# Performance work log

Measured on AMD Instinct MI355X. Metric: run time of the kernel, lower is better.

## Reference

```python
import jax, jax.numpy as jnp
import numpy as np


def setup_inputs() -> dict:
    key = jax.random.key(0)
    k1, k2, k3, k4, k5, k6 = jax.random.split(key, 6)
    Ne, dim_in, dim_out, B, Nr, E = 100000, 128, 128, 4, 8, 200000
    return {
        "H": jax.random.normal(k1, (Ne, dim_in), dtype=jnp.float32),
        "A": jax.random.uniform(k2, (Nr, B), dtype=jnp.float32),
        "V": jax.random.uniform(k3, (B, dim_in, dim_out), dtype=jnp.float32),
        "edge_row": jax.random.randint(k4, (Nr, E), 0, Ne, dtype=jnp.int32),
        "edge_col": jax.random.randint(k5, (Nr, E), 0, Ne, dtype=jnp.int32),
        "edge_val": jax.random.uniform(k6, (Nr, E), dtype=jnp.float32),
    }


def reference(H, A, V, edge_row, edge_col, edge_val):
    # W = einsum('rb,bio->rio', A, V): basis-decomposed relation weights
    Ne = H.shape[0]
    Nr = A.shape[0]
    W = jnp.einsum('rb,bio->rio', A, V)            # [Nr, dim_in, dim_out]
    HxW = jnp.einsum('ni,rio->rno', H, W)          # [Nr, Ne, dim_out]
    # sparse T_r @ HxW_r: gather source rows (cols of T), scale by values,
    # scatter-add into destination rows. Done for all relations at once.
    msgs = HxW[jnp.arange(Nr)[:, None], edge_col] * edge_val[..., None]  # [Nr, E, dim_out]
    out = jax.ops.segment_sum(
        msgs.reshape(-1, msgs.shape[-1]),
        edge_row.reshape(-1),
        num_segments=Ne,
    )  # sum over relations folded into one segment_sum
    return out
```

## Files before the change

### kernel.cpp

```cpp
#include <hip/hip_runtime.h>

typedef __attribute__((ext_vector_type(8))) short short8;
typedef __attribute__((ext_vector_type(4))) float floatx4;

constexpr int DIM   = 128;
constexpr int NB    = 4;
constexpr int NR    = 8;
constexpr int BROWS = 512;
constexpr int BCAP  = 16384;

static __device__ __forceinline__ unsigned short f2bf(float f) {
    unsigned int u = __float_as_uint(f);
    u += 0x7FFFu + ((u >> 16) & 1u);
    return (unsigned short)(u >> 16);
}
static __device__ __forceinline__ float bf_lo(unsigned int h) {
    return __uint_as_float(h << 16);
}
static __device__ __forceinline__ float bf_hi(unsigned int h) {
    return __uint_as_float(h & 0xFFFF0000u);
}

__global__ __launch_bounds__(256) void build_vfrag(
    const float* __restrict__ V, unsigned short* __restrict__ VfragG)
{
    int idx  = blockIdx.x * 256 + threadIdx.x;
    int lane = idx & 63;
    int ks   = (idx >> 6) & 3;
    int ot   = (idx >> 8) & 7;
    int b    = idx >> 11;

    int o  = ot * 16 + (lane & 15);
    int kb = ks * 32 + (lane >> 4) * 8;

    short8 v;
#pragma unroll
    for (int j = 0; j < 8; ++j)
        v[j] = (short)f2bf(V[((size_t)b * DIM + kb + j) * DIM + o]);
    *reinterpret_cast<short8*>(VfragG + (size_t)idx * 8) = v;
}

__global__ __launch_bounds__(256) void build_wfrag(
    const float* __restrict__ A, const float* __restrict__ V,
    unsigned short* __restrict__ Wfrag)
{
    int idx  = blockIdx.x * 256 + threadIdx.x;
    int lane = idx & 63;
    int ks   = (idx >> 6) & 3;
    int ot   = (idx >> 8) & 7;
    int r    = idx >> 11;

    int o     = ot * 16 + (lane & 15);
    int kbase = ks * 32 + (lane >> 4) * 8;

    float a0 = A[r * NB + 0], a1 = A[r * NB + 1];
    float a2 = A[r * NB + 2], a3 = A[r * NB + 3];

    short8 v;
#pragma unroll
    for (int j = 0; j < 8; ++j) {
        int k = kbase + j;
        float w = a0 * V[(0 * DIM + k) * DIM + o]
                + a1 * V[(1 * DIM + k) * DIM + o]
                + a2 * V[(2 * DIM + k) * DIM + o]
                + a3 * V[(3 * DIM + k) * DIM + o];
        v[j] = (short)f2bf(w);
    }
    *reinterpret_cast<short8*>(Wfrag + (size_t)idx * 8) = v;
}

__global__ __launch_bounds__(256) void h_to_bf(
    const float* __restrict__ H, unsigned short* __restrict__ Hbf, int n8)
{
    int i = blockIdx.x * 256 + threadIdx.x;
    if (i >= n8) return;
    const float4* hp = reinterpret_cast<const float4*>(H) + (size_t)i * 2;
    float4 f0 = hp[0];
    float4 f1 = hp[1];
    short8 v;
    v[0] = (short)f2bf(f0.x); v[1] = (short)f2bf(f0.y);
    v[2] = (short)f2bf(f0.z); v[3] = (short)f2bf(f0.w);
    v[4] = (short)f2bf(f1.x); v[5] = (short)f2bf(f1.y);
    v[6] = (short)f2bf(f1.z); v[7] = (short)f2bf(f1.w);
    *reinterpret_cast<short8*>(Hbf + (size_t)i * 8) = v;
}

__global__ __launch_bounds__(256) void bucket_scatter(
    const int* __restrict__ erow, const int* __restrict__ ecol,
    const float* __restrict__ eval, int* __restrict__ bcnt,
    int2* __restrict__ sorted1, int n, int E, int chunk)
{
    __shared__ int cnt[256];
    __shared__ int base[256];
    int t = threadIdx.x;
    cnt[t] = 0;
    __syncthreads();

    int s = blockIdx.x * chunk;
    int e = s + chunk; if (e > n) e = n;

    for (int i = s + t; i < e; i += 256)
        atomicAdd(&cnt[erow[i] >> 9], 1);
    __syncthreads();

    int c = cnt[t];
    base[t] = (c > 0) ? atomicAdd(&bcnt[t], c) : 0;
    cnt[t] = 0;
    __syncthreads();

    for (int i = s + t; i < e; i += 256) {
        int row = erow[i];
        int bkt = row >> 9;
        int rank = atomicAdd(&cnt[bkt], 1);
        int r = (int)((unsigned)i / (unsigned)E);
        int2 m;
        m.x = ((row & (BROWS - 1)) << 20) | (r << 17) | ecol[i];
        m.y = __float_as_int(eval[i]);
        sorted1[(size_t)bkt * BCAP + base[bkt] + rank] = m;
    }
}

__global__ __launch_bounds__(256) void bucket_scan(
    const int* __restrict__ bcnt, int* __restrict__ bstart,
    int* __restrict__ rowStart, int nbuc, int Ne)
{
    __shared__ int sd[256];
    int t = threadIdx.x;
    int c = (t < nbuc) ? bcnt[t] : 0;
    sd[t] = c; __syncthreads();
#pragma unroll
    for (int off = 1; off < 256; off <<= 1) {
        int v = (t >= off) ? sd[t - off] : 0;
        __syncthreads();
        sd[t] += v;
        __syncthreads();
    }
    if (t < nbuc) bstart[t] = sd[t] - c;
    if (t == nbuc - 1) rowStart[Ne] = sd[t];
}

__global__ __launch_bounds__(256) void bucket_sort(
    const int2* __restrict__ sorted1, const int* __restrict__ bcnt,
    const int* __restrict__ bstart, int* __restrict__ rowStart,
    int2* __restrict__ sorted, int Ne)
{
    __shared__ int hcnt[BROWS];
    __shared__ int hoff[BROWS];
    int b = blockIdx.x;
    int t = threadIdx.x;
    hcnt[t] = 0; hcnt[t + 256] = 0;
    __syncthreads();

    int n = bcnt[b];
    const int2* src = sorted1 + (size_t)b * BCAP;

    for (int i = t; i < n; i += 256)
        atomicAdd(&hcnt[(unsigned)src[i].x >> 20], 1);
    __syncthreads();

    if (t == 0) {
        int run = 0;
#pragma unroll 8
        for (int j = 0; j < BROWS; ++j) { hoff[j] = run; run += hcnt[j]; }
    }
    __syncthreads();

    int bs = bstart[b];
    int rs = b * BROWS;
    int nr = Ne - rs; if (nr > BROWS) nr = BROWS;
    for (int j = t; j < nr; j += 256)
        rowStart[rs + j] = bs + hoff[j];

    hcnt[t] = 0; hcnt[t + 256] = 0;
    __syncthreads();

    for (int i = t; i < n; i += 256) {
        int2 m = src[i];
        int lr = (unsigned)m.x >> 20;
        int pos = bs + hoff[lr] + atomicAdd(&hcnt[lr], 1);
        sorted[pos] = m;
    }
}

__global__ __launch_bounds__(256) void agg_kernel(
    const unsigned short* __restrict__ Hbf,
    const int*  __restrict__ rowStart,
    const int2* __restrict__ sorted,
    const float* __restrict__ Aw,
    unsigned short* __restrict__ AggT, int Ne)
{
    int tid  = threadIdx.x;
    int wid  = __builtin_amdgcn_readfirstlane(blockIdx.x * 4 + (tid >> 6));
    if (wid >= Ne) return;
    int lane = tid & 63;

    int s = __builtin_amdgcn_readfirstlane(rowStart[wid]);
    int e = __builtin_amdgcn_readfirstlane(rowStart[wid + 1]);

    const float4* Af = reinterpret_cast<const float4*>(Aw);

    float2 acc[4];
#pragma unroll
    for (int b = 0; b < 4; ++b) { acc[b].x = 0.f; acc[b].y = 0.f; }

    int i = s;
    for (; i + 8 <= e; i += 8) {
        int kk[8];
        float vv[8];
        unsigned int hh[8];
#pragma unroll
        for (int u = 0; u < 8; ++u) {
            int2 m = sorted[i + u];
            kk[u] = __builtin_amdgcn_readfirstlane(m.x);
            vv[u] = __uint_as_float(__builtin_amdgcn_readfirstlane(m.y));
        }
#pragma unroll
        for (int u = 0; u < 8; ++u)
            hh[u] = reinterpret_cast<const unsigned int*>(
                Hbf + (size_t)(kk[u] & 0x1FFFF) * DIM)[lane];
#pragma unroll
        for (int u = 0; u < 8; ++u) {
            float4 a = Af[((unsigned)kk[u] >> 17) & 7];
            float hx = bf_lo(hh[u]), hy = bf_hi(hh[u]);
            float s0 = vv[u] * a.x, s1 = vv[u] * a.y;
            float s2 = vv[u] * a.z, s3 = vv[u] * a.w;
            acc[0].x += s0 * hx; acc[0].y += s0 * hy;
            acc[1].x += s1 * hx; acc[1].y += s1 * hy;
            acc[2].x += s2 * hx; acc[2].y += s2 * hy;
            acc[3].x += s3 * hx; acc[3].y += s3 * hy;
        }
    }
    for (; i < e; ++i) {
        int2 m = sorted[i];
        int k = __builtin_amdgcn_readfirstlane(m.x);
        float v = __uint_as_float(__builtin_amdgcn_readfirstlane(m.y));
        unsigned int h = reinterpret_cast<const unsigned int*>(
            Hbf + (size_t)(k & 0x1FFFF) * DIM)[lane];
        float4 a = Af[((unsigned)k >> 17) & 7];
        float hx = bf_lo(h), hy = bf_hi(h);
        float s0 = v * a.x, s1 = v * a.y, s2 = v * a.z, s3 = v * a.w;
        acc[0].x += s0 * hx; acc[0].y += s0 * hy;
        acc[1].x += s1 * hx; acc[1].y += s1 * hy;
        acc[2].x += s2 * hx; acc[2].y += s2 * hy;
        acc[3].x += s3 * hx; acc[3].y += s3 * hy;
    }

    int t = wid >> 4, r = wid & 15;
    size_t base = (size_t)t * 8192 + (size_t)r * 32
                + (size_t)(lane >> 4) * 512
                + (size_t)((lane >> 2) & 3) * 8
                + (size_t)(lane & 3) * 2;
    unsigned short* arow = AggT + base;
#pragma unroll
    for (int b = 0; b < 4; ++b) {
        unsigned int pk = (unsigned int)f2bf(acc[b].x)
                        | ((unsigned int)f2bf(acc[b].y) << 16);
        *reinterpret_cast<unsigned int*>(arow + b * 2048) = pk;
    }
}

__global__ __launch_bounds__(512) void vgemm_kernel(
    const unsigned short* __restrict__ AggT,
    const unsigned short* __restrict__ VfragG,
    float* __restrict__ out, int Ne, int nTiles)
{
    __shared__ short8 ldsV[4096];
    int half = (blockIdx.x >> 3) & 1;
    int blk  = ((blockIdx.x >> 4) << 3) | (blockIdx.x & 7);
    int nblk = gridDim.x >> 1;
    int tid  = threadIdx.x;

    for (int i = tid; i < 4096; i += 512) {
        int lane = i & 63, ks = (i >> 6) & 3, otl = (i >> 8) & 3, b = i >> 10;
        int gi = ((b * 8 + half * 4 + otl) * 4 + ks) * 64 + lane;
        ldsV[i] = reinterpret_cast<const short8*>(VfragG)[gi];
    }
    __syncthreads();

    int wave = tid >> 6;
    int lane = tid & 63;
    int quad = lane >> 4, l15 = lane & 15;

    int wgid = blk * 8 + wave;
    int nw   = nblk * 8;

    const short8* AggV = reinterpret_cast<const short8*>(AggT);

    for (int tile = wgid; tile < nTiles; tile += nw) {
        int node = tile * 16 + l15;

        const short8* bp = AggV + (size_t)tile * 1024 + l15 * 4 + quad;
        short8 bf[16];
#pragma unroll
        for (int b = 0; b < 4; ++b)
#pragma unroll
            for (int ks = 0; ks < 4; ++ks)
                bf[b * 4 + ks] = bp[b * 256 + ks * 64];

        floatx4 acc[4];
#pragma unroll
        for (int o = 0; o < 4; ++o) acc[o] = (floatx4){0.f, 0.f, 0.f, 0.f};

#pragma unroll
        for (int b = 0; b < 4; ++b)
#pragma unroll
            for (int ks = 0; ks < 4; ++ks)
#pragma unroll
                for (int otl = 0; otl < 4; ++otl)
                    acc[otl] = __builtin_amdgcn_mfma_f32_16x16x32_bf16(
                        ldsV[((b * 4 + otl) * 4 + ks) * 64 + lane],
                        bf[b * 4 + ks], acc[otl], 0, 0, 0);

        if (node < Ne) {
            float* orow = out + (size_t)node * DIM + half * 64;
#pragma unroll
            for (int otl = 0; otl < 4; ++otl) {
                float4 st;
                st.x = acc[otl][0]; st.y = acc[otl][1];
                st.z = acc[otl][2]; st.w = acc[otl][3];
                *reinterpret_cast<float4*>(orow + otl * 16 + quad * 4) = st;
            }
        }
    }
}

__global__ __launch_bounds__(256) void rgcn_main(
    const unsigned short* __restrict__ Hbf,
    const unsigned short* __restrict__ Wfrag,
    const int*   __restrict__ erow,
    const int*   __restrict__ ecol,
    const float* __restrict__ eval,
    float*       __restrict__ out,
    int E, int groups_per_rel, int waves_per_rel)
{
    int wid  = blockIdx.x * 4 + (threadIdx.x >> 6);
    int lane = threadIdx.x & 63;
    int r    = wid & 7;
    int wr   = wid >> 3;
    int quad = lane >> 4;
    int l15  = lane & 15;

    short8 b[8][4];
    {
        const short8* wp = reinterpret_cast<const short8*>(
            Wfrag + (size_t)r * 16384);
#pragma unroll
        for (int ot = 0; ot < 8; ++ot)
#pragma unroll
            for (int ks = 0; ks < 4; ++ks)
                b[ot][ks] = wp[(ot * 4 + ks) * 64 + lane];
    }

    for (int g = wr; g < groups_per_rel; g += waves_per_rel) {
        int ebase = r * E + g * 16;
        int   colv = ecol[ebase + l15];
        int   rowv = erow[ebase + l15];
        float valv = eval[ebase + l15];

        short8 a[4];
        const unsigned short* hp = Hbf + (size_t)colv * DIM + quad * 8;
#pragma unroll
        for (int ks = 0; ks < 4; ++ks)
            a[ks] = *reinterpret_cast<const short8*>(hp + ks * 32);

        floatx4 acc[8];
#pragma unroll
        for (int ot = 0; ot < 8; ++ot) acc[ot] = (floatx4){0.f, 0.f, 0.f, 0.f};
#pragma unroll
        for (int ot = 0; ot < 8; ++ot)
#pragma unroll
            for (int ks = 0; ks < 4; ++ks)
                acc[ot] = __builtin_amdgcn_mfma_f32_16x16x32_bf16(
                    a[ks], b[ot][ks], acc[ot], 0, 0, 0);

        int   row4[4];
        float val4[4];
#pragma unroll
        for (int reg = 0; reg < 4; ++reg) {
            int src  = quad * 4 + reg;
            row4[reg] = __shfl(rowv, src, 64);
            val4[reg] = __shfl(valv, src, 64);
        }
#pragma unroll
        for (int ot = 0; ot < 8; ++ot)
#pragma unroll
            for (int reg = 0; reg < 4; ++reg) {
                float m = acc[ot][reg] * val4[reg];
                atomicAdd(out + (size_t)row4[reg] * DIM + ot * 16 + l15, m);
            }
    }
}

extern "C" void kernel_launch(void* const* d_in, const int* in_sizes, int n_in,
                              void* d_out, int out_size, void* d_ws, size_t ws_size,
                              hipStream_t stream)
{
    const float* H    = (const float*)d_in[0];
    const float* A    = (const float*)d_in[1];
    const float* V    = (const float*)d_in[2];
    const int*   erow = (const int*)d_in[3];
    const int*   ecol = (const int*)d_in[4];
    const float* eval = (const float*)d_in[5];
    float* out = (float*)d_out;

    int Ne    = in_sizes[0] / DIM;
    int NEtot = in_sizes[3];
    int E     = NEtot / NR;

    auto al = [](size_t x) { return (x + 255) & ~(size_t)255; };

    int nbuc = (Ne + BROWS - 1) / BROWS;
    int nTiles = (Ne + 15) / 16;

    size_t offHbf    = 0;
    size_t offVfrag  = offHbf    + al((size_t)Ne * DIM * 2);
    size_t offWfrag  = offVfrag  + al((size_t)8192 * 16);
    size_t offAgg    = offWfrag  + al((size_t)16384 * 16);
    size_t offRow    = offAgg    + al((size_t)nTiles * 16384);
    size_t offBcnt   = offRow    + al(((size_t)Ne + 2) * 4);
    size_t offBstart = offBcnt   + al((size_t)256 * 4);
    size_t offSort   = offBstart + al((size_t)256 * 4);
    size_t total     = offSort   + al((size_t)NEtot * 8);

    char* ws = (char*)d_ws;
    unsigned short* Hbf    = (unsigned short*)(ws + offHbf);
    unsigned short* VfragG = (unsigned short*)(ws + offVfrag);
    unsigned short* Wfrag  = (unsigned short*)(ws + offWfrag);

    int n8 = Ne * DIM / 8;
    h_to_bf<<<(n8 + 255) / 256, 256, 0, stream>>>(H, Hbf, n8);

    if (ws_size < total) {
        build_wfrag<<<64, 256, 0, stream>>>(A, V, Wfrag);
        hipMemsetAsync(d_out, 0, (size_t)Ne * DIM * sizeof(float), stream);
        int blocks = 4096;
        int waves_per_rel = blocks * 4 / NR;
        int groups_per_rel = E / 16;
        rgcn_main<<<blocks, 256, 0, stream>>>(Hbf, Wfrag, erow, ecol, eval, out,
                                              E, groups_per_rel, waves_per_rel);
        return;
    }

    unsigned short* AggT     = (unsigned short*)(ws + offAgg);
    int2*           sorted1  = (int2*)(ws + offAgg);
    int*            rowStart = (int*)(ws + offRow);
    int*            bcnt     = (int*)(ws + offBcnt);
    int*            bstart   = (int*)(ws + offBstart);
    int2*           sorted   = (int2*)(ws + offSort);

    build_vfrag<<<32, 256, 0, stream>>>(V, VfragG);

    hipMemsetAsync(bcnt, 0, 256 * 4, stream);
    int sblocks = 512;
    int chunk   = (NEtot + sblocks - 1) / sblocks;
    bucket_scatter<<<sblocks, 256, 0, stream>>>(erow, ecol, eval, bcnt,
                                                sorted1, NEtot, E, chunk);
    bucket_scan<<<1, 256, 0, stream>>>(bcnt, bstart, rowStart, nbuc, Ne);
    bucket_sort<<<nbuc, 256, 0, stream>>>(sorted1, bcnt, bstart, rowStart,
                                          sorted, Ne);

    agg_kernel<<<(Ne + 3) / 4, 256, 0, stream>>>(Hbf, rowStart, sorted, A,
                                                 AggT, Ne);

    vgemm_kernel<<<512, 512, 0, stream>>>(AggT, VfragG, out, Ne, nTiles);
}
```

Baseline: 327.9 us.

## Fuse bucket scan into sort and double-buffer gathers in aggregation

The single-block bucket_scan kernel is removed. Each bucket_sort block now recomputes the 256-entry prefix sum of bucket counts in shared memory, which saves one kernel launch and the round trip through the bstart buffer. The agg_kernel main loop is software-pipelined with two register sets, so the next 8 edges' index and H gathers are issued before the FMAs for the current 8. The accumulators use 2-wide float vectors so the compiler can emit packed FMA. This costs more registers (possibly lower occupancy) and redundant scan work in every sort block.

Result: no change. 324.6 us (-1.0%).

```diff
diff --git a/kernel.cpp b/kernel.cpp
--- a/kernel.cpp
+++ b/kernel.cpp
@@ -2,6 +2,7 @@
 
 typedef __attribute__((ext_vector_type(8))) short short8;
 typedef __attribute__((ext_vector_type(4))) float floatx4;
+typedef __attribute__((ext_vector_type(2))) float floatx2;
 
 constexpr int DIM   = 128;
 constexpr int NB    = 4;
@@ -120,14 +121,19 @@
     }
 }
 
-__global__ __launch_bounds__(256) void bucket_scan(
-    const int* __restrict__ bcnt, int* __restrict__ bstart,
-    int* __restrict__ rowStart, int nbuc, int Ne)
-{
+__global__ __launch_bounds__(256) void bucket_sort(
+    const int2* __restrict__ sorted1, const int* __restrict__ bcnt,
+    int* __restrict__ rowStart, int2* __restrict__ sorted, int Ne, int nbuc)
+{
+    __shared__ int hcnt[BROWS];
+    __shared__ int hoff[BROWS];
     __shared__ int sd[256];
+    int b = blockIdx.x;
     int t = threadIdx.x;
+    hcnt[t] = 0; hcnt[t + 256] = 0;
     int c = (t < nbuc) ? bcnt[t] : 0;
-    sd[t] = c; __syncthreads();
+    sd[t] = c;
+    __syncthreads();
 #pragma unroll
     for (int off = 1; off < 256; off <<= 1) {
         int v = (t >= off) ? sd[t - off] : 0;
@@ -135,23 +141,10 @@
         sd[t] += v;
         __syncthreads();
     }
-    if (t < nbuc) bstart[t] = sd[t] - c;
-    if (t == nbuc - 1) rowStart[Ne] = sd[t];
-}
-
-__global__ __launch_bounds__(256) void bucket_sort(
-    const int2* __restrict__ sorted1, const int* __restrict__ bcnt,
-    const int* __restrict__ bstart, int* __restrict__ rowStart,
-    int2* __restrict__ sorted, int Ne)
-{
-    __shared__ int hcnt[BROWS];
-    __shared__ int hoff[BROWS];
-    int b = blockIdx.x;
-    int t = threadIdx.x;
-    hcnt[t] = 0; hcnt[t + 256] = 0;
-    __syncthreads();
-
-    int n = bcnt[b];
+    if (b == 0 && t == nbuc - 1) rowStart[Ne] = sd[t];
+
+    int n  = bcnt[b];
+    int bs = sd[b] - n;
     const int2* src = sorted1 + (size_t)b * BCAP;
 
     for (int i = t; i < n; i += 256)
@@ -165,7 +158,6 @@
     }
     __syncthreads();
 
-    int bs = bstart[b];
     int rs = b * BROWS;
     int nr = Ne - rs; if (nr > BROWS) nr = BROWS;
     for (int j = t; j < nr; j += 256)
@@ -181,6 +173,31 @@
         sorted[pos] = m;
     }
 }
+
+#define AGG_LOAD8(kk, vv, hh, base)                                          \
+    _Pragma("unroll")                                                        \
+    for (int u = 0; u < 8; ++u) {                                            \
+        int2 m = sorted[(base) + u];                                         \
+        kk[u] = __builtin_amdgcn_readfirstlane(m.x);                         \
+        vv[u] = __uint_as_float(__builtin_amdgcn_readfirstlane(m.y));        \
+    }                                                                        \
+    _Pragma("unroll")                                                        \
+    for (int u = 0; u < 8; ++u)                                              \
+        hh[u] = reinterpret_cast<const unsigned int*>(                       \
+            Hbf + (size_t)(kk[u] & 0x1FFFF) * DIM)[lane];
+
+#define AGG_FMA8(kk, vv, hh)                                                 \
+    _Pragma("unroll")                                                        \
+    for (int u = 0; u < 8; ++u) {                                            \
+        float4 a = Af[((unsigned)kk[u] >> 17) & 7];                          \
+        floatx2 h; h[0] = bf_lo(hh[u]); h[1] = bf_hi(hh[u]);                 \
+        float s0 = vv[u] * a.x, s1 = vv[u] * a.y;                            \
+        float s2 = vv[u] * a.z, s3 = vv[u] * a.w;                            \
+        acc[0] += (floatx2){s0, s0} * h;                                     \
+        acc[1] += (floatx2){s1, s1} * h;                                     \
+        acc[2] += (floatx2){s2, s2} * h;                                     \
+        acc[3] += (floatx2){s3, s3} * h;                                     \
+    }
 
 __global__ __launch_bounds__(256) void agg_kernel(
     const unsigned short* __restrict__ Hbf,
@@ -199,50 +216,40 @@
 
     const float4* Af = reinterpret_cast<const float4*>(Aw);
 
-    float2 acc[4];
-#pragma unroll
-    for (int b = 0; b < 4; ++b) { acc[b].x = 0.f; acc[b].y = 0.f; }
+    floatx2 acc[4];
+#pragma unroll
+    for (int b = 0; b < 4; ++b) acc[b] = (floatx2){0.f, 0.f};
 
     int i = s;
-    for (; i + 8 <= e; i += 8) {
-        int kk[8];
-        float vv[8];
-        unsigned int hh[8];
-#pragma unroll
-        for (int u = 0; u < 8; ++u) {
-            int2 m = sorted[i + u];
-            kk[u] = __builtin_amdgcn_readfirstlane(m.x);
-            vv[u] = __uint_as_float(__builtin_amdgcn_readfirstlane(m.y));
-        }
-#pragma unroll
-        for (int u = 0; u < 8; ++u)
-            hh[u] = reinterpret_cast<const unsigned int*>(
-                Hbf + (size_t)(kk[u] & 0x1FFFF) * DIM)[lane];
-#pragma unroll
-        for (int u = 0; u < 8; ++u) {
-            float4 a = Af[((unsigned)kk[u] >> 17) & 7];
-            float hx = bf_lo(hh[u]), hy = bf_hi(hh[u]);
-            float s0 = vv[u] * a.x, s1 = vv[u] * a.y;
-            float s2 = vv[u] * a.z, s3 = vv[u] * a.w;
-            acc[0].x += s0 * hx; acc[0].y += s0 * hy;
-            acc[1].x += s1 * hx; acc[1].y += s1 * hy;
-            acc[2].x += s2 * hx; acc[2].y += s2 * hy;
-            acc[3].x += s3 * hx; acc[3].y += s3 * hy;
+    if (i + 8 <= e) {
+        int kkA[8], kkB[8];
+        float vvA[8], vvB[8];
+        unsigned int hhA[8], hhB[8];
+        AGG_LOAD8(kkA, vvA, hhA, i); i += 8;
+        for (;;) {
+            if (i + 8 <= e) {
+                AGG_LOAD8(kkB, vvB, hhB, i); i += 8;
+                AGG_FMA8(kkA, vvA, hhA);
+            } else { AGG_FMA8(kkA, vvA, hhA); break; }
+            if (i + 8 <= e) {
+                AGG_LOAD8(kkA, vvA, hhA, i); i += 8;
+                AGG_FMA8(kkB, vvB, hhB);
+            } else { AGG_FMA8(kkB, vvB, hhB); break; }
         }
     }
     for (; i < e; ++i) {
         int2 m = sorted[i];
         int k = __builtin_amdgcn_readfirstlane(m.x);
         float v = __uint_as_float(__builtin_amdgcn_readfirstlane(m.y));
-        unsigned int h = reinterpret_cast<const unsigned int*>(
+        unsigned int hu = reinterpret_cast<const unsigned int*>(
             Hbf + (size_t)(k & 0x1FFFF) * DIM)[lane];
         float4 a = Af[((unsigned)k >> 17) & 7];
-        float hx = bf_lo(h), hy = bf_hi(h);
+        floatx2 h; h[0] = bf_lo(hu); h[1] = bf_hi(hu);
         float s0 = v * a.x, s1 = v * a.y, s2 = v * a.z, s3 = v * a.w;
-        acc[0].x += s0 * hx; acc[0].y += s0 * hy;
-        acc[1].x += s1 * hx; acc[1].y += s1 * hy;
-        acc[2].x += s2 * hx; acc[2].y += s2 * hy;
-        acc[3].x += s3 * hx; acc[3].y += s3 * hy;
+        acc[0] += (floatx2){s0, s0} * h;
+        acc[1] += (floatx2){s1, s1} * h;
+        acc[2] += (floatx2){s2, s2} * h;
+        acc[3] += (floatx2){s3, s3} * h;
     }
 
     int t = wid >> 4, r = wid & 15;
@@ -253,8 +260,8 @@
     unsigned short* arow = AggT + base;
 #pragma unroll
     for (int b = 0; b < 4; ++b) {
-        unsigned int pk = (unsigned int)f2bf(acc[b].x)
-                        | ((unsigned int)f2bf(acc[b].y) << 16);
+        unsigned int pk = (unsigned int)f2bf(acc[b][0])
+                        | ((unsigned int)f2bf(acc[b][1]) << 16);
         *reinterpret_cast<unsigned int*>(arow + b * 2048) = pk;
     }
 }
@@ -418,8 +425,7 @@
     size_t offAgg    = offWfrag  + al((size_t)16384 * 16);
     size_t offRow    = offAgg    + al((size_t)nTiles * 16384);
     size_t offBcnt   = offRow    + al(((size_t)Ne + 2) * 4);
-    size_t offBstart = offBcnt   + al((size_t)256 * 4);
-    size_t offSort   = offBstart + al((size_t)256 * 4);
+    size_t offSort   = offBcnt   + al((size_t)256 * 4);
     size_t total     = offSort   + al((size_t)NEtot * 8);
 
     char* ws = (char*)d_ws;
@@ -445,7 +451,6 @@
     int2*           sorted1  = (int2*)(ws + offAgg);
     int*            rowStart = (int*)(ws + offRow);
     int*            bcnt     = (int*)(ws + offBcnt);
-    int*            bstart   = (int*)(ws + offBstart);
     int2*           sorted   = (int2*)(ws + offSort);
 
     build_vfrag<<<32, 256, 0, stream>>>(V, VfragG);
@@ -455,9 +460,8 @@
     int chunk   = (NEtot + sblocks - 1) / sblocks;
     bucket_scatter<<<sblocks, 256, 0, stream>>>(erow, ecol, eval, bcnt,
                                                 sorted1, NEtot, E, chunk);
-    bucket_scan<<<1, 256, 0, stream>>>(bcnt, bstart, rowStart, nbuc, Ne);
-    bucket_sort<<<nbuc, 256, 0, stream>>>(sorted1, bcnt, bstart, rowStart,
-                                          sorted, Ne);
+    bucket_sort<<<nbuc, 256, 0, stream>>>(sorted1, bcnt, rowStart,
+                                          sorted, Ne, nbuc);
 
     agg_kernel<<<(Ne + 3) / 4, 256, 0, stream>>>(Hbf, rowStart, sorted, A,
                                                  AggT, Ne);
```
